# Optimization experiments

Hardware: AMD Instinct MI355X
Metric: run time of the kernel (lower is better)

## Reference

```python
import jax, jax.numpy as jnp
import numpy as np

P = 256        # number of graph pairs
LMAX = 32      # max graph size (padded to LMAX+1 incl. virtual node)
F = 2048       # num_input_features
E = 256        # embedding_dim
INF = 10000.0


def _lengths():
    i = np.arange(P)
    len_s = 8 + (i % 25)
    len_t = 8 + ((7 * i + 3) % 25)
    return len_s.astype(np.int32), len_t.astype(np.int32)


def setup_inputs() -> dict:
    key = jax.random.key(0)
    ks = jax.random.split(key, 6)
    len_s_np, len_t_np = _lengths()
    Ns, Nt = int(len_s_np.sum()), int(len_t_np.sum())
    x_s = jax.random.normal(ks[0], (Ns, F), jnp.float32)
    x_t = jax.random.normal(ks[1], (Nt, F), jnp.float32)
    W1 = jax.random.normal(ks[2], (E, F), jnp.float32) / np.float32(np.sqrt(F))
    b1 = jnp.zeros((E,), jnp.float32)
    W2 = jax.random.normal(ks[3], (E, E), jnp.float32) / np.float32(np.sqrt(E))
    b2 = jnp.zeros((E,), jnp.float32)
    virtual_embedding = jax.random.uniform(ks[4], (F,), jnp.float32)
    return {"x_s": x_s, "x_t": x_t, "W1": W1, "b1": b1, "W2": W2, "b2": b2,
            "virtual_embedding": virtual_embedding,
            "len_s": jnp.asarray(len_s_np), "len_t": jnp.asarray(len_t_np)}


def _embed(x, W1, b1, W2, b2):
    # nn.Sequential(Linear, Dropout(eval=identity), ReLU, Linear, ReLU)
    h = jax.nn.relu(x @ W1.T + b1)
    return jax.nn.relu(h @ W2.T + b2)


def _safe_cdist(a, b):
    # a: [P,L,E], b: [P,L,E] -> [P,L,L] Euclidean, grad-safe at 0
    sq = (jnp.sum(a * a, -1)[:, :, None] + jnp.sum(b * b, -1)[:, None, :]
          - 2.0 * jnp.einsum('pid,pjd->pij', a, b))
    sq = jnp.maximum(sq, 0.0)
    pos = sq > 0
    return jnp.where(pos, jnp.sqrt(jnp.where(pos, sq, 1.0)), 0.0)


def _pad_embed(emb, virtual_e, lens):
    # ragged [N,E] -> padded [P,LMAX+1,E]; slot lens[p] (and beyond) = virtual
    pos = jnp.arange(LMAX + 1)
    off = jnp.cumsum(lens) - lens                       # exclusive prefix sum
    idx = off[:, None] + jnp.minimum(pos[None, :], lens[:, None] - 1)
    mask = pos[None, :] < lens[:, None]
    return jnp.where(mask[..., None], emb[idx], virtual_e[None, None, :])


def _edit_costs(x_s, x_t, W1, b1, W2, b2, virtual_embedding, len_s, len_t):
    emb_s = _embed(x_s, W1, b1, W2, b2)
    emb_t = _embed(x_t, W1, b1, W2, b2)
    ve = _embed(virtual_embedding[None, :], W1, b1, W2, b2)[0]
    A = _pad_embed(emb_s, ve, len_s)                    # [P,L+1,E]
    B = _pad_embed(emb_t, ve, len_t)
    d = _safe_cdist(A, B)                               # [P,L+1,L+1]
    pos = jnp.arange(LMAX + 1)
    valid = ((pos[None, :, None] <= len_s[:, None, None]) &
             (pos[None, None, :] <= len_t[:, None, None]))
    tot = jnp.sum(jnp.where(valid, d, 0.0), axis=(1, 2))
    scale = (len_s * len_t).astype(d.dtype) / tot
    return jnp.where(valid, d * scale[:, None, None], 0.0), valid


def _lap_jv(C):
    # Jonker-Volgenant / e-maxx Hungarian for square cost matrix; returns col of each row
    C = np.asarray(C, dtype=np.float64)
    n = C.shape[0]
    u = np.zeros(n + 1)
    v = np.zeros(n + 1)
    p = np.zeros(n + 1, dtype=np.int64)
    way = np.zeros(n + 1, dtype=np.int64)
    for i in range(1, n + 1):
        p[0] = i
        j0 = 0
        minv = np.full(n + 1, np.inf)
        used = np.zeros(n + 1, dtype=bool)
        while True:
            used[j0] = True
            i0 = p[j0]
            cur = C[i0 - 1, :] - u[i0] - v[1:]
            upd = (~used[1:]) & (cur < minv[1:])
            minv[1:][upd] = cur[upd]
            way[1:][upd] = j0
            masked = np.where(used[1:], np.inf, minv[1:])
            j1 = int(np.argmin(masked)) + 1
            delta = masked[j1 - 1]
            u[p[used]] += delta
            v[used] -= delta
            minv[1:][~used[1:]] -= delta
            j0 = j1
            if p[j0] == 0:
                break
        while j0:
            j1 = way[j0]
            p[j0] = p[j1]
            j0 = j1
    row_of_col = p[1:] - 1
    col_of_row = np.empty(n, dtype=np.int64)
    col_of_row[row_of_col] = np.arange(n)
    return col_of_row


def _lsape_align(ec, n, m):
    # LSAPE expansion identical to GEDModelHomology.lsape
    N = n + m
    C = np.zeros((N, N))
    C[:n, :m] = ec[:n, :m]
    C[n:, :m] = INF
    C[:n, m:] = INF
    C[np.arange(n, n + m), np.arange(m)] = ec[n, :m]
    C[np.arange(n), np.arange(m, m + n)] = ec[:n, m]
    C[~np.isfinite(C)] = INF
    p = _lap_jv(C)
    q = np.arange(N)
    align = np.zeros((n + 1, m + 1), dtype=np.int32)
    align[np.minimum(q, n), np.minimum(p, m)] = 1
    align[-1, -1] = 0
    return align


def _alignments(costs_np, len_s_np, len_t_np):
    out = np.zeros((costs_np.shape[0], LMAX + 1, LMAX + 1), dtype=np.int32)
    for pr in range(costs_np.shape[0]):
        n, m = int(len_s_np[pr]), int(len_t_np[pr])
        out[pr, :n + 1, :m + 1] = _lsape_align(costs_np[pr, :n + 1, :m + 1], n, m)
    return out


def reference(x_s, x_t, W1, b1, W2, b2, virtual_embedding, len_s, len_t):
    costs, _ = _edit_costs(x_s, x_t, W1, b1, W2, b2, virtual_embedding, len_s, len_t)
    aligns = jnp.asarray(_alignments(np.asarray(costs),
                                     np.asarray(len_s), np.asarray(len_t)))
    geds = (jnp.sum(aligns.astype(costs.dtype) * costs, axis=(1, 2))
            / (len_s + len_t).astype(costs.dtype))
    return aligns, costs, geds
```

## Files before the change

### kernel.cpp

```cpp
#include <hip/hip_runtime.h>
#include <math.h>

#define LMAXP1 33
#define EDIM   256
#define FBIG   3.0e38f

typedef _Float16 half8 __attribute__((ext_vector_type(8)));
typedef float    f32x4 __attribute__((ext_vector_type(4)));

__device__ inline unsigned pk2h(_Float16 a, _Float16 b) {
    union { _Float16 h[2]; unsigned u; } q; q.h[0] = a; q.h[1] = b; return q.u;
}

#define ASTR 20
__global__ __launch_bounds__(256)
void k_gemm_splitk(const float* __restrict__ S0, int n0,
                   const float* __restrict__ S1, int n1,
                   const float* __restrict__ S2,
                   const float* __restrict__ W,
                   float* __restrict__ Part, int Mtot, int K, int kchunk,
                   const float* __restrict__ bias) {
    __shared__ alignas(16) unsigned AsH[64 * ASTR],  AsL[64 * ASTR];
    __shared__ alignas(16) unsigned BsH[256 * ASTR], BsL[256 * ASTR];
    const int tid = threadIdx.x;
    const int m0  = blockIdx.x * 64;
    const int ks  = blockIdx.z;
    const int kb  = ks * kchunk;
    const int ke  = (kb + kchunk < K) ? kb + kchunk : K;

    const int sar = tid >> 2, sak = (tid & 3) << 3;
    const int gr  = m0 + sar;
    const float* srow = nullptr;
    if (gr < n0)            srow = S0 + (size_t)gr * K;
    else if (gr < n0 + n1)  srow = S1 + (size_t)(gr - n0) * K;
    else if (gr < Mtot)     srow = S2;

    const int lane = tid & 63, wv = tid >> 6;
    const int wc = wv << 6;
    const int lr = lane & 15, lq = lane >> 4;

    f32x4 acc[4][4] = {};

    for (int k0 = kb; k0 < ke; k0 += 32) {
        {
            float x[8];
            if (srow) {
                const float4 f0 = *(const float4*)(srow + k0 + sak + 0);
                const float4 f1 = *(const float4*)(srow + k0 + sak + 4);
                x[0]=f0.x; x[1]=f0.y; x[2]=f0.z; x[3]=f0.w;
                x[4]=f1.x; x[5]=f1.y; x[6]=f1.z; x[7]=f1.w;
            } else {
                #pragma unroll
                for (int j = 0; j < 8; ++j) x[j] = 0.f;
            }
            unsigned uh[4], ul[4];
            #pragma unroll
            for (int j = 0; j < 4; ++j) {
                const _Float16 h0 = (_Float16)x[2*j],   h1 = (_Float16)x[2*j+1];
                const _Float16 l0 = (_Float16)(x[2*j]   - (float)h0);
                const _Float16 l1 = (_Float16)(x[2*j+1] - (float)h1);
                uh[j] = pk2h(h0, h1); ul[j] = pk2h(l0, l1);
            }
            *(uint4*)(AsH + sar * ASTR + (sak >> 1)) = make_uint4(uh[0],uh[1],uh[2],uh[3]);
            *(uint4*)(AsL + sar * ASTR + (sak >> 1)) = make_uint4(ul[0],ul[1],ul[2],ul[3]);
        }
        #pragma unroll
        for (int it = 0; it < 4; ++it) {
            const int idx = tid + it * 256;
            const int br = idx >> 2, bk = (idx & 3) << 3;
            const float* wr_ = W + (size_t)br * K + k0 + bk;
            const float4 f0 = *(const float4*)(wr_ + 0);
            const float4 f1 = *(const float4*)(wr_ + 4);
            const float y[8] = {f0.x,f0.y,f0.z,f0.w,f1.x,f1.y,f1.z,f1.w};
            unsigned uh[4], ul[4];
            #pragma unroll
            for (int j = 0; j < 4; ++j) {
                const float a0 = y[2*j] * 1024.0f, a1 = y[2*j+1] * 1024.0f;
                const _Float16 h0 = (_Float16)a0, h1 = (_Float16)a1;
                const _Float16 l0 = (_Float16)(a0 - (float)h0);
                const _Float16 l1 = (_Float16)(a1 - (float)h1);
                uh[j] = pk2h(h0, h1); ul[j] = pk2h(l0, l1);
            }
            *(uint4*)(BsH + br * ASTR + (bk >> 1)) = make_uint4(uh[0],uh[1],uh[2],uh[3]);
            *(uint4*)(BsL + br * ASTR + (bk >> 1)) = make_uint4(ul[0],ul[1],ul[2],ul[3]);
        }
        __syncthreads();

        half8 bhv[4], blv[4];
        #pragma unroll
        for (int ct = 0; ct < 4; ++ct) {
            const int br = wc + ct * 16 + lr;
            bhv[ct] = *(const half8*)((const char*)BsH + br * 80 + lq * 16);
            blv[ct] = *(const half8*)((const char*)BsL + br * 80 + lq * 16);
        }
        #pragma unroll
        for (int rt = 0; rt < 4; ++rt) {
            const int ar = rt * 16 + lr;
            const half8 ah = *(const half8*)((const char*)AsH + ar * 80 + lq * 16);
            const half8 al = *(const half8*)((const char*)AsL + ar * 80 + lq * 16);
            #pragma unroll
            for (int ct = 0; ct < 4; ++ct) {
                acc[rt][ct] = __builtin_amdgcn_mfma_f32_16x16x32_f16(ah, bhv[ct], acc[rt][ct], 0, 0, 0);
                acc[rt][ct] = __builtin_amdgcn_mfma_f32_16x16x32_f16(ah, blv[ct], acc[rt][ct], 0, 0, 0);
                acc[rt][ct] = __builtin_amdgcn_mfma_f32_16x16x32_f16(al, bhv[ct], acc[rt][ct], 0, 0, 0);
            }
        }
        __syncthreads();
    }

    float* pout = Part + (size_t)ks * ((size_t)Mtot * EDIM);
    const float sc = 1.0f / 1024.0f;
    #pragma unroll
    for (int rt = 0; rt < 4; ++rt) {
        #pragma unroll
        for (int r = 0; r < 4; ++r) {
            const int grr = m0 + rt * 16 + lq * 4 + r;
            if (grr >= Mtot) continue;
            #pragma unroll
            for (int ct = 0; ct < 4; ++ct) {
                const int gc = wc + ct * 16 + lr;
                float vv = acc[rt][ct][r] * sc;
                if (bias) vv = fmaxf(vv + bias[gc], 0.0f);
                pout[(size_t)grr * EDIM + gc] = vv;
            }
        }
    }
}

__global__ __launch_bounds__(256)
void k_reduce_bias_relu(const float* __restrict__ Part,
                        const float* __restrict__ bias,
                        float* __restrict__ C, int S, size_t MN4) {
    const size_t i = (size_t)blockIdx.x * blockDim.x + threadIdx.x;
    const size_t stride = (size_t)gridDim.x * blockDim.x;
    const size_t MN = MN4 * 4;
    for (size_t i4 = i; i4 < MN4; i4 += stride) {
        float4 s = ((const float4*)Part)[i4];
        for (int z = 1; z < S; ++z)
            { const float4 q = ((const float4*)(Part + (size_t)z * MN))[i4];
              s.x += q.x; s.y += q.y; s.z += q.z; s.w += q.w; }
        const float4 b = ((const float4*)bias)[i4 & 63];
        s.x = fmaxf(s.x + b.x, 0.f); s.y = fmaxf(s.y + b.y, 0.f);
        s.z = fmaxf(s.z + b.z, 0.f); s.w = fmaxf(s.w + b.w, 0.f);
        ((float4*)C)[i4] = s;
    }
}

__global__ __launch_bounds__(256)
void k_embed_gemm(const float* __restrict__ S0, int n0,
                  const float* __restrict__ S1, int n1,
                  const float* __restrict__ S2,
                  const float* __restrict__ W, const float* __restrict__ bias,
                  float* __restrict__ C, int Mtot, int K) {
    __shared__ alignas(16) float As[16][68];
    __shared__ alignas(16) float Bs[16][68];
    const int tid  = threadIdx.x;
    const int tx   = tid & 15, ty = tid >> 4;
    const int m0   = blockIdx.x * 64, nc0 = blockIdx.y * 64;
    const int lrow = tid >> 2;
    const int lk4  = (tid & 3) << 2;

    const int gr = m0 + lrow;
    const float* srow = nullptr;
    if (gr < n0)            srow = S0 + (size_t)gr * K;
    else if (gr < n0 + n1)  srow = S1 + (size_t)(gr - n0) * K;
    else if (gr < Mtot)     srow = S2;
    const float* wrow = W + (size_t)(nc0 + lrow) * K;

    float acc[4][4] = {};
    for (int k0 = 0; k0 < K; k0 += 16) {
        float4 va = make_float4(0.f, 0.f, 0.f, 0.f);
        if (srow) va = *(const float4*)(srow + k0 + lk4);
        const float4 vb = *(const float4*)(wrow + k0 + lk4);
        As[lk4+0][lrow] = va.x; As[lk4+1][lrow] = va.y;
        As[lk4+2][lrow] = va.z; As[lk4+3][lrow] = va.w;
        Bs[lk4+0][lrow] = vb.x; Bs[lk4+1][lrow] = vb.y;
        Bs[lk4+2][lrow] = vb.z; Bs[lk4+3][lrow] = vb.w;
        __syncthreads();
        #pragma unroll
        for (int kk = 0; kk < 16; ++kk) {
            const float4 a4 = *(const float4*)&As[kk][ty << 2];
            const float4 b4 = *(const float4*)&Bs[kk][tx << 2];
            const float av[4] = {a4.x, a4.y, a4.z, a4.w};
            const float bv[4] = {b4.x, b4.y, b4.z, b4.w};
            #pragma unroll
            for (int i2 = 0; i2 < 4; ++i2)
                #pragma unroll
                for (int j2 = 0; j2 < 4; ++j2)
                    acc[i2][j2] = fmaf(av[i2], bv[j2], acc[i2][j2]);
        }
        __syncthreads();
    }
    #pragma unroll
    for (int i2 = 0; i2 < 4; ++i2) {
        const int grr = m0 + (ty << 2) + i2;
        if (grr >= Mtot) continue;
        #pragma unroll
        for (int j2 = 0; j2 < 4; ++j2) {
            const int gc = nc0 + (tx << 2) + j2;
            const float vv = acc[i2][j2] + bias[gc];
            C[(size_t)grr * EDIM + gc] = fmaxf(vv, 0.0f);
        }
    }
}

#define CSTR 36
__global__ __launch_bounds__(256)
void k_costs(const float* __restrict__ Emb, const int* __restrict__ len_s,
             const int* __restrict__ len_t, int Ns, int Nt,
             float* __restrict__ costs) {
    __shared__ alignas(16) unsigned Ah[34 * CSTR], Al[34 * CSTR];
    __shared__ alignas(16) unsigned Bh[34 * CSTR], Bl[34 * CSTR];
    __shared__ float dtile[LMAXP1 * LMAXP1];
    __shared__ float na[LMAXP1], nb[LMAXP1];
    __shared__ float red[256];
    __shared__ float s_scale;
    const int p = blockIdx.x, tid = threadIdx.x;
    const int n = len_s[p], m = len_t[p];
    int offs = 0, offt = 0;
    for (int j = 0; j < p; ++j) { offs += len_s[j]; offt += len_t[j]; }
    const int veRow = Ns + Nt;
    const int tbase = Ns + offt;

    const int lane = tid & 63, wv = tid >> 6;
    const int lr = lane & 15, lq = lane >> 4;

    if (tid <= n) {
        const float* src = (tid < n) ? (Emb + (size_t)(offs + tid) * EDIM)
                                     : (Emb + (size_t)veRow * EDIM);
        const float4* a4 = (const float4*)src;
        float s = 0.f;
        for (int k = 0; k < 64; ++k) {
            const float4 a = a4[k];
            s = fmaf(a.x, a.x, s); s = fmaf(a.y, a.y, s);
            s = fmaf(a.z, a.z, s); s = fmaf(a.w, a.w, s);
        }
        na[tid] = s;
    } else if (tid >= 64 && tid - 64 <= m) {
        const int j = tid - 64;
        const float* src = (j < m) ? (Emb + (size_t)(tbase + j) * EDIM)
                                   : (Emb + (size_t)veRow * EDIM);
        const float4* b4 = (const float4*)src;
        float s = 0.f;
        for (int k = 0; k < 64; ++k) {
            const float4 b = b4[k];
            s = fmaf(b.x, b.x, s); s = fmaf(b.y, b.y, s);
            s = fmaf(b.z, b.z, s); s = fmaf(b.w, b.w, s);
        }
        nb[j] = s;
    }

    f32x4 g0 = {}, g1 = {}, g2 = {};
    const int t0 = wv, t1 = wv + 4, t2 = wv + 8;

    for (int k0 = 0; k0 < EDIM; k0 += 64) {
        for (int idx = tid; idx < 34 * 16; idx += 256) {
            const int r = idx >> 4, c4 = idx & 15;
            float4 va = make_float4(0.f,0.f,0.f,0.f), vb = va;
            if (r < n)       va = *(const float4*)(Emb + (size_t)(offs + r) * EDIM + k0 + c4*4);
            else if (r == n) va = *(const float4*)(Emb + (size_t)veRow * EDIM + k0 + c4*4);
            if (r < m)       vb = *(const float4*)(Emb + (size_t)(tbase + r) * EDIM + k0 + c4*4);
            else if (r == m) vb = *(const float4*)(Emb + (size_t)veRow * EDIM + k0 + c4*4);
            const float xa[4] = {va.x, va.y, va.z, va.w};
            const float xb[4] = {vb.x, vb.y, vb.z, vb.w};
            unsigned ah_[2], al_[2], bh_[2], bl_[2];
            #pragma unroll
            for (int j = 0; j < 2; ++j) {
                const _Float16 h0 = (_Float16)xa[2*j],   h1 = (_Float16)xa[2*j+1];
                const _Float16 l0 = (_Float16)(xa[2*j]   - (float)h0);
                const _Float16 l1 = (_Float16)(xa[2*j+1] - (float)h1);
                ah_[j] = pk2h(h0, h1); al_[j] = pk2h(l0, l1);
                const _Float16 g0_ = (_Float16)xb[2*j],   g1_ = (_Float16)xb[2*j+1];
                const _Float16 m0_ = (_Float16)(xb[2*j]   - (float)g0_);
                const _Float16 m1_ = (_Float16)(xb[2*j+1] - (float)g1_);
                bh_[j] = pk2h(g0_, g1_); bl_[j] = pk2h(m0_, m1_);
            }
            const int uo = r * CSTR + c4 * 2;
            *(uint2*)(Ah + uo) = make_uint2(ah_[0], ah_[1]);
            *(uint2*)(Al + uo) = make_uint2(al_[0], al_[1]);
            *(uint2*)(Bh + uo) = make_uint2(bh_[0], bh_[1]);
            *(uint2*)(Bl + uo) = make_uint2(bl_[0], bl_[1]);
        }
        __syncthreads();

        #pragma unroll
        for (int kf = 0; kf < 2; ++kf) {
#define GRAM_TILE(T, G) { \
            const int tr_ = (T) / 3, tc_ = (T) % 3;                              \
            const int ar_ = tr_ * 16 + lr, br_ = tc_ * 16 + lr;                  \
            const half8 ah = *(const half8*)((const char*)Ah + ar_*144 + kf*64 + lq*16); \
            const half8 al = *(const half8*)((const char*)Al + ar_*144 + kf*64 + lq*16); \
            const half8 bh = *(const half8*)((const char*)Bh + br_*144 + kf*64 + lq*16); \
            const half8 bl = *(const half8*)((const char*)Bl + br_*144 + kf*64 + lq*16); \
            G = __builtin_amdgcn_mfma_f32_16x16x32_f16(ah, bh, G, 0, 0, 0);      \
            G = __builtin_amdgcn_mfma_f32_16x16x32_f16(ah, bl, G, 0, 0, 0);      \
            G = __builtin_amdgcn_mfma_f32_16x16x32_f16(al, bh, G, 0, 0, 0); }
            GRAM_TILE(t0, g0)
            GRAM_TILE(t1, g1)
            if (wv == 0) GRAM_TILE(t2, g2)
#undef GRAM_TILE
        }
        __syncthreads();
    }

#define DTILE_OUT(T, G) { \
    const int tr_ = (T) / 3, tc_ = (T) % 3;                                      \
    _Pragma("unroll")                                                            \
    for (int r = 0; r < 4; ++r) {                                                \
        const int i_ = tr_ * 16 + lq * 4 + r, j_ = tc_ * 16 + lr;                \
        if (i_ <= n && j_ <= m) {                                                \
            const float sq = fmaxf(na[i_] + nb[j_] - 2.0f * G[r], 0.0f);         \
            dtile[i_ * LMAXP1 + j_] = (sq > 0.0f) ? sqrtf(sq) : 0.0f;            \
        } } }
    DTILE_OUT(t0, g0)
    DTILE_OUT(t1, g1)
    if (wv == 0) DTILE_OUT(t2, g2)
#undef DTILE_OUT
    __syncthreads();

    float lsum = 0.f;
    const int m1 = m + 1;
    const int cells = (n + 1) * m1;
    for (int c = tid; c < cells; c += 256) {
        const int i = c / m1, j = c - i * m1;
        lsum += dtile[i * LMAXP1 + j];
    }
    red[tid] = lsum;
    __syncthreads();
    for (int s = 128; s > 0; s >>= 1) {
        if (tid < s) red[tid] += red[tid + s];
        __syncthreads();
    }
    if (tid == 0) s_scale = (float)(n * m) / red[0];
    __syncthreads();
    const float scale = s_scale;
    for (int idx = tid; idx < LMAXP1 * LMAXP1; idx += 256) {
        const int i = idx / LMAXP1, j = idx - i * LMAXP1;
        const float v = (i <= n && j <= m) ? dtile[i * LMAXP1 + j] * scale : 0.0f;
        costs[(size_t)p * (LMAXP1 * LMAXP1) + idx] = v;
    }
}

__device__ inline int rdlane_i(int v, int l) { return __builtin_amdgcn_readlane(v, l); }
__device__ inline float rdlane_f(float v, int l) {
    return __int_as_float(__builtin_amdgcn_readlane(__float_as_int(v), l));
}
__device__ inline unsigned wave_umin64(unsigned x) {
#define DPPMINU(ctrl) { unsigned t_ = (unsigned)__builtin_amdgcn_update_dpp(  \
        (int)x, (int)x, (ctrl), 0xf, 0xf, false);                             \
        x = (t_ < x) ? t_ : x; }
    DPPMINU(0xB1)
    DPPMINU(0x4E)
    DPPMINU(0x141)
    DPPMINU(0x140)
    DPPMINU(0x142)
    DPPMINU(0x143)
#undef DPPMINU
    return (unsigned)__builtin_amdgcn_readlane((int)x, 63);
}

__global__ __launch_bounds__(64)
void k_lap(const float* __restrict__ costs, const int* __restrict__ len_s,
           const int* __restrict__ len_t, float* __restrict__ aligns,
           float* __restrict__ geds) {
    __shared__ float ec[LMAXP1 * LMAXP1];
    __shared__ float Ms[33 * 64];
    const int p = blockIdx.x, lane = threadIdx.x;
    const int n = len_s[p], m = len_t[p];
    const float* cp = costs + (size_t)p * (LMAXP1 * LMAXP1);
    for (int idx = lane; idx < LMAXP1 * LMAXP1; idx += 64) ec[idx] = cp[idx];
    __syncthreads();

    const bool swp = (n > m);
    const int R  = swp ? n : m;
    const int S_ = swp ? m : n;
    const bool vec = (lane >= 1 && lane <= R);

    for (int r = 1; r <= R; ++r) {
        float cv = FBIG;
        const int i0b = r - 1, j0b = lane - 1;
        if (vec) {
            if (!swp) {
                const float ins = ec[n * LMAXP1 + j0b];
                cv = (i0b < S_)
                   ? fminf(ec[i0b * LMAXP1 + j0b], ec[i0b * LMAXP1 + m] + ins)
                   : ins;
            } else {
                const float ins = ec[j0b * LMAXP1 + m];
                cv = (i0b < S_)
                   ? fminf(ec[j0b * LMAXP1 + i0b], ec[n * LMAXP1 + i0b] + ins)
                   : ins;
            }
        }
        Ms[(r << 6) + lane] = cv;
    }
    __syncthreads();

    float v_l = 0.0f;
    int amin_l = 0;
    if (vec) {
        float best = FBIG;
        for (int r = 1; r <= R; ++r) {
            const float c = Ms[(r << 6) + lane];
            if (c < best) { best = c; amin_l = r; }
        }
        v_l = best;
    }
    int p_l = 0;
    unsigned long long rowfree = ((1ull << R) - 1ull) << 1;
    for (int j = 1; j <= R; ++j) {
        const int ai = rdlane_i(amin_l, j);
        if ((rowfree >> ai) & 1ull) {
            if (lane == j) p_l = ai;
            rowfree &= ~(1ull << ai);
        }
    }

    float ucol = 0.0f, minv_l = FBIG;
    int way_l = 0;

    for (int i = 1; i <= R; ++i) {
        if (!((rowfree >> i) & 1ull)) continue;
        if (lane == 0) { p_l = i; ucol = 0.0f; }
        minv_l = FBIG;
        int used_l = 0;
        int j0 = 0, i0 = i;
        float u_i0 = 0.0f;
        while (true) {
            if (lane == j0) used_l = 1;
            const float cur = Ms[(i0 << 6) + lane] - u_i0 - v_l;
            const bool unused = vec && !used_l;
            if (unused && cur < minv_l) { minv_l = cur; way_l = j0; }
            const float mval = unused ? fmaxf(minv_l, 0.0f) : FBIG;
            const unsigned key = (__float_as_uint(mval) & ~63u) | (unsigned)lane;
            const unsigned kmin = wave_umin64(key);
            const int j1 = (int)(kmin & 63u);
            const float delta = rdlane_f(minv_l, j1);
            if (used_l) { ucol += delta; v_l -= delta; }
            if (unused) minv_l -= delta;
            j0 = j1;
            i0 = rdlane_i(p_l, j1);
            u_i0 = rdlane_f(ucol, j1);
            if (i0 == 0) break;
        }
        int jj = j0;
        while (jj != 0) {
            const int   j1a = rdlane_i(way_l, jj);
            const int   pn  = rdlane_i(p_l, j1a);
            const float un  = rdlane_f(ucol, j1a);
            if (lane == jj) { p_l = pn; ucol = un; }
            jj = j1a;
        }
    }

    float* ap = aligns + (size_t)p * (LMAXP1 * LMAXP1);
    for (int idx = lane; idx < LMAXP1 * LMAXP1; idx += 64) ap[idx] = 0.0f;
    __syncthreads();
    float gedv = 0.0f;
    if (vec) {
        const int i0b = p_l - 1;
        const int j0b = lane - 1;
        if (!swp) {
            if (i0b < S_) {
                const float sub = ec[i0b * LMAXP1 + j0b];
                const float alt = ec[i0b * LMAXP1 + m] + ec[n * LMAXP1 + j0b];
                if (sub <= alt) { ap[i0b * LMAXP1 + j0b] = 1.0f; gedv = sub; }
                else { ap[i0b * LMAXP1 + m] = 1.0f;
                       ap[n * LMAXP1 + j0b] = 1.0f;
                       gedv = alt; }
            } else {
                ap[n * LMAXP1 + j0b] = 1.0f;
                gedv = ec[n * LMAXP1 + j0b];
            }
        } else {
            if (i0b < S_) {
                const float sub = ec[j0b * LMAXP1 + i0b];
                const float alt = ec[n * LMAXP1 + i0b] + ec[j0b * LMAXP1 + m];
                if (sub <= alt) { ap[j0b * LMAXP1 + i0b] = 1.0f; gedv = sub; }
                else { ap[n * LMAXP1 + i0b] = 1.0f;
                       ap[j0b * LMAXP1 + m] = 1.0f;
                       gedv = alt; }
            } else {
                ap[j0b * LMAXP1 + m] = 1.0f;
                gedv = ec[j0b * LMAXP1 + m];
            }
        }
    }
    #pragma unroll
    for (int off = 32; off > 0; off >>= 1) gedv += __shfl_xor(gedv, off);
    if (lane == 0) geds[p] = gedv / (float)(n + m);
}

extern "C" void kernel_launch(void* const* d_in, const int* in_sizes, int n_in,
                              void* d_out, int out_size, void* d_ws, size_t ws_size,
                              hipStream_t stream) {
    const float* x_s = (const float*)d_in[0];
    const float* x_t = (const float*)d_in[1];
    const float* W1  = (const float*)d_in[2];
    const float* b1  = (const float*)d_in[3];
    const float* W2  = (const float*)d_in[4];
    const float* b2  = (const float*)d_in[5];
    const float* ve  = (const float*)d_in[6];
    const int* len_s = (const int*)d_in[7];
    const int* len_t = (const int*)d_in[8];
    const int P    = in_sizes[7];
    const int Ns   = in_sizes[0] / 2048;
    const int Nt   = in_sizes[1] / 2048;
    const int Mtot = Ns + Nt + 1;
    const size_t MN  = (size_t)Mtot * EDIM;

    float* H    = (float*)d_ws;
    float* Emb  = H + MN;
    float* Part = Emb + MN;

    int S = 1;
    if (ws_size >= (2 + 4) * MN * sizeof(float)) S = 4;
    else if (ws_size >= (2 + 2) * MN * sizeof(float)) S = 2;

    float* out_aligns = (float*)d_out;
    float* out_costs  = out_aligns + (size_t)P * LMAXP1 * LMAXP1;
    float* out_geds   = out_costs  + (size_t)P * LMAXP1 * LMAXP1;

    const dim3 b256(256);
    const int gx64 = (Mtot + 63) / 64;

    if (S > 1) {
        k_gemm_splitk<<<dim3(gx64, 1, S), b256, 0, stream>>>(
            x_s, Ns, x_t, Nt, ve, W1, Part, Mtot, 2048, 2048 / S, nullptr);
        const size_t MN4 = MN / 4;
        const int rblocks = (int)((MN4 + 255) / 256) < 2048
                          ? (int)((MN4 + 255) / 256) : 2048;
        k_reduce_bias_relu<<<dim3(rblocks), b256, 0, stream>>>(Part, b1, H, S, MN4);
        k_gemm_splitk<<<dim3(gx64, 1, 1), b256, 0, stream>>>(
            H, Mtot, nullptr, 0, nullptr, W2, Emb, Mtot, 256, 256, b2);
    } else {
        k_embed_gemm<<<dim3(gx64, 4), b256, 0, stream>>>(
            x_s, Ns, x_t, Nt, ve, W1, b1, H, Mtot, 2048);
        k_embed_gemm<<<dim3(gx64, 4), b256, 0, stream>>>(
            H, Mtot, nullptr, 0, nullptr, W2, b2, Emb, Mtot, 256);
    }
    k_costs<<<dim3(P), b256, 0, stream>>>(Emb, len_s, len_t, Ns, Nt, out_costs);
    k_lap<<<dim3(P), dim3(64), 0, stream>>>(out_costs, len_s, len_t, out_aligns, out_geds);
}
```

Before: 180.1 us.

## Pre-split weights and hidden activations into fp16 hi/lo buffers before GEMMs

Adds a conversion kernel that splits W1 and W2 once per call into packed fp16 high/low halves. The split-K GEMM now loads these directly instead of converting weights inside every block. The reduce kernel also emits the hidden layer as fp16 hi/lo, so a new dedicated GEMM for layer 2 consumes it without reconverting. This removes redundant per-block conversion work at the cost of two extra launches and extra workspace traffic.

```diff
diff --git a/kernel.cpp b/kernel.cpp
--- a/kernel.cpp
+++ b/kernel.cpp
@@ -10,6 +10,19 @@
 
 __device__ inline unsigned pk2h(_Float16 a, _Float16 b) {
     union { _Float16 h[2]; unsigned u; } q; q.h[0] = a; q.h[1] = b; return q.u;
+}
+
+__global__ __launch_bounds__(256)
+void k_convw(const float* __restrict__ W, unsigned* __restrict__ Wh,
+             unsigned* __restrict__ Wl, int npairs) {
+    const int stride = gridDim.x * blockDim.x;
+    for (int i = blockIdx.x * blockDim.x + threadIdx.x; i < npairs; i += stride) {
+        const float a0 = W[2*i] * 1024.0f, a1 = W[2*i+1] * 1024.0f;
+        const _Float16 h0 = (_Float16)a0, h1 = (_Float16)a1;
+        const _Float16 l0 = (_Float16)(a0 - (float)h0);
+        const _Float16 l1 = (_Float16)(a1 - (float)h1);
+        Wh[i] = pk2h(h0, h1); Wl[i] = pk2h(l0, l1);
+    }
 }
 
 #define ASTR 20
@@ -17,9 +30,8 @@
 void k_gemm_splitk(const float* __restrict__ S0, int n0,
                    const float* __restrict__ S1, int n1,
                    const float* __restrict__ S2,
-                   const float* __restrict__ W,
-                   float* __restrict__ Part, int Mtot, int K, int kchunk,
-                   const float* __restrict__ bias) {
+                   const unsigned* __restrict__ Wh, const unsigned* __restrict__ Wl,
+                   float* __restrict__ Part, int Mtot, int K, int kchunk) {
     __shared__ alignas(16) unsigned AsH[64 * ASTR],  AsL[64 * ASTR];
     __shared__ alignas(16) unsigned BsH[256 * ASTR], BsL[256 * ASTR];
     const int tid = threadIdx.x;
@@ -68,21 +80,9 @@
         for (int it = 0; it < 4; ++it) {
             const int idx = tid + it * 256;
             const int br = idx >> 2, bk = (idx & 3) << 3;
-            const float* wr_ = W + (size_t)br * K + k0 + bk;
-            const float4 f0 = *(const float4*)(wr_ + 0);
-            const float4 f1 = *(const float4*)(wr_ + 4);
-            const float y[8] = {f0.x,f0.y,f0.z,f0.w,f1.x,f1.y,f1.z,f1.w};
-            unsigned uh[4], ul[4];
-            #pragma unroll
-            for (int j = 0; j < 4; ++j) {
-                const float a0 = y[2*j] * 1024.0f, a1 = y[2*j+1] * 1024.0f;
-                const _Float16 h0 = (_Float16)a0, h1 = (_Float16)a1;
-                const _Float16 l0 = (_Float16)(a0 - (float)h0);
-                const _Float16 l1 = (_Float16)(a1 - (float)h1);
-                uh[j] = pk2h(h0, h1); ul[j] = pk2h(l0, l1);
-            }
-            *(uint4*)(BsH + br * ASTR + (bk >> 1)) = make_uint4(uh[0],uh[1],uh[2],uh[3]);
-            *(uint4*)(BsL + br * ASTR + (bk >> 1)) = make_uint4(ul[0],ul[1],ul[2],ul[3]);
+            const size_t uoff = (size_t)br * (K >> 1) + ((k0 + bk) >> 1);
+            *(uint4*)(BsH + br * ASTR + (bk >> 1)) = *(const uint4*)(Wh + uoff);
+            *(uint4*)(BsL + br * ASTR + (bk >> 1)) = *(const uint4*)(Wl + uoff);
         }
         __syncthreads();
 
@@ -117,12 +117,8 @@
             const int grr = m0 + rt * 16 + lq * 4 + r;
             if (grr >= Mtot) continue;
             #pragma unroll
-            for (int ct = 0; ct < 4; ++ct) {
-                const int gc = wc + ct * 16 + lr;
-                float vv = acc[rt][ct][r] * sc;
-                if (bias) vv = fmaxf(vv + bias[gc], 0.0f);
-                pout[(size_t)grr * EDIM + gc] = vv;
-            }
+            for (int ct = 0; ct < 4; ++ct)
+                pout[(size_t)grr * EDIM + wc + ct * 16 + lr] = acc[rt][ct][r] * sc;
         }
     }
 }
@@ -130,7 +126,8 @@
 __global__ __launch_bounds__(256)
 void k_reduce_bias_relu(const float* __restrict__ Part,
                         const float* __restrict__ bias,
-                        float* __restrict__ C, int S, size_t MN4) {
+                        unsigned* __restrict__ Hh, unsigned* __restrict__ Hl,
+                        int S, size_t MN4) {
     const size_t i = (size_t)blockIdx.x * blockDim.x + threadIdx.x;
     const size_t stride = (size_t)gridDim.x * blockDim.x;
     const size_t MN = MN4 * 4;
@@ -142,7 +139,91 @@
         const float4 b = ((const float4*)bias)[i4 & 63];
         s.x = fmaxf(s.x + b.x, 0.f); s.y = fmaxf(s.y + b.y, 0.f);
         s.z = fmaxf(s.z + b.z, 0.f); s.w = fmaxf(s.w + b.w, 0.f);
-        ((float4*)C)[i4] = s;
+        const _Float16 hx = (_Float16)s.x, hy = (_Float16)s.y;
+        const _Float16 hz = (_Float16)s.z, hw = (_Float16)s.w;
+        Hh[i4*2+0] = pk2h(hx, hy);
+        Hh[i4*2+1] = pk2h(hz, hw);
+        Hl[i4*2+0] = pk2h((_Float16)(s.x - (float)hx), (_Float16)(s.y - (float)hy));
+        Hl[i4*2+1] = pk2h((_Float16)(s.z - (float)hz), (_Float16)(s.w - (float)hw));
+    }
+}
+
+__global__ __launch_bounds__(256)
+void k_gemm_f16(const unsigned* __restrict__ Ah, const unsigned* __restrict__ Al,
+                const unsigned* __restrict__ Wh, const unsigned* __restrict__ Wl,
+                const float* __restrict__ bias,
+                float* __restrict__ C, int Mtot, int K) {
+    __shared__ alignas(16) unsigned AsH[64 * ASTR],  AsL[64 * ASTR];
+    __shared__ alignas(16) unsigned BsH[256 * ASTR], BsL[256 * ASTR];
+    const int tid = threadIdx.x;
+    const int m0  = blockIdx.x * 64;
+
+    const int sar = tid >> 2, sak = (tid & 3) << 3;
+    const int gr  = m0 + sar;
+    const bool arow = (gr < Mtot);
+
+    const int lane = tid & 63, wv = tid >> 6;
+    const int wc = wv << 6;
+    const int lr = lane & 15, lq = lane >> 4;
+
+    f32x4 acc[4][4] = {};
+
+    for (int k0 = 0; k0 < K; k0 += 32) {
+        {
+            uint4 vh = make_uint4(0,0,0,0), vl = vh;
+            if (arow) {
+                const size_t uoff = (size_t)gr * (K >> 1) + ((k0 + sak) >> 1);
+                vh = *(const uint4*)(Ah + uoff);
+                vl = *(const uint4*)(Al + uoff);
+            }
+            *(uint4*)(AsH + sar * ASTR + (sak >> 1)) = vh;
+            *(uint4*)(AsL + sar * ASTR + (sak >> 1)) = vl;
+        }
+        #pragma unroll
+        for (int it = 0; it < 4; ++it) {
+            const int idx = tid + it * 256;
+            const int br = idx >> 2, bk = (idx & 3) << 3;
+            const size_t uoff = (size_t)br * (K >> 1) + ((k0 + bk) >> 1);
+            *(uint4*)(BsH + br * ASTR + (bk >> 1)) = *(const uint4*)(Wh + uoff);
+            *(uint4*)(BsL + br * ASTR + (bk >> 1)) = *(const uint4*)(Wl + uoff);
+        }
+        __syncthreads();
+
+        half8 bhv[4], blv[4];
+        #pragma unroll
+        for (int ct = 0; ct < 4; ++ct) {
+            const int br = wc + ct * 16 + lr;
+            bhv[ct] = *(const half8*)((const char*)BsH + br * 80 + lq * 16);
+            blv[ct] = *(const half8*)((const char*)BsL + br * 80 + lq * 16);
+        }
+        #pragma unroll
+        for (int rt = 0; rt < 4; ++rt) {
+            const int ar = rt * 16 + lr;
+            const half8 ah = *(const half8*)((const char*)AsH + ar * 80 + lq * 16);
+            const half8 al = *(const half8*)((const char*)AsL + ar * 80 + lq * 16);
+            #pragma unroll
+            for (int ct = 0; ct < 4; ++ct) {
+                acc[rt][ct] = __builtin_amdgcn_mfma_f32_16x16x32_f16(ah, bhv[ct], acc[rt][ct], 0, 0, 0);
+                acc[rt][ct] = __builtin_amdgcn_mfma_f32_16x16x32_f16(ah, blv[ct], acc[rt][ct], 0, 0, 0);
+                acc[rt][ct] = __builtin_amdgcn_mfma_f32_16x16x32_f16(al, bhv[ct], acc[rt][ct], 0, 0, 0);
+            }
+        }
+        __syncthreads();
+    }
+
+    const float sc = 1.0f / 1024.0f;
+    #pragma unroll
+    for (int rt = 0; rt < 4; ++rt) {
+        #pragma unroll
+        for (int r = 0; r < 4; ++r) {
+            const int grr = m0 + rt * 16 + lq * 4 + r;
+            if (grr >= Mtot) continue;
+            #pragma unroll
+            for (int ct = 0; ct < 4; ++ct) {
+                const int gc = wc + ct * 16 + lr;
+                C[(size_t)grr * EDIM + gc] = fmaxf(acc[rt][ct][r] * sc + bias[gc], 0.0f);
+            }
+        }
     }
 }
 
@@ -509,14 +590,6 @@
     const int Mtot = Ns + Nt + 1;
     const size_t MN  = (size_t)Mtot * EDIM;
 
-    float* H    = (float*)d_ws;
-    float* Emb  = H + MN;
-    float* Part = Emb + MN;
-
-    int S = 1;
-    if (ws_size >= (2 + 4) * MN * sizeof(float)) S = 4;
-    else if (ws_size >= (2 + 2) * MN * sizeof(float)) S = 2;
-
     float* out_aligns = (float*)d_out;
     float* out_costs  = out_aligns + (size_t)P * LMAXP1 * LMAXP1;
     float* out_geds   = out_costs  + (size_t)P * LMAXP1 * LMAXP1;
@@ -524,21 +597,44 @@
     const dim3 b256(256);
     const int gx64 = (Mtot + 63) / 64;
 
-    if (S > 1) {
+    const size_t fixed = MN  + 2 * 262144 + 2 * 32768;
+    int S = 0;
+    if (ws_size >= (4 * MN + fixed) * sizeof(float)) S = 4;
+    else if (ws_size >= (2 * MN + fixed) * sizeof(float)) S = 2;
+
+    if (S > 0) {
+        float* Part = (float*)d_ws;
+        float* Emb  = Part;
+        unsigned* Hh  = (unsigned*)(Part + (size_t)S * MN);
+        unsigned* Hl  = Hh + MN / 2;
+        unsigned* W1h = Hl + MN / 2;
+        unsigned* W1l = W1h + 262144;
+        unsigned* W2h = W1l + 262144;
+        unsigned* W2l = W2h + 32768;
+
+        k_convw<<<dim3(1024), b256, 0, stream>>>(W1, W1h, W1l, 262144);
+        k_convw<<<dim3(128),  b256, 0, stream>>>(W2, W2h, W2l, 32768);
+
         k_gemm_splitk<<<dim3(gx64, 1, S), b256, 0, stream>>>(
-            x_s, Ns, x_t, Nt, ve, W1, Part, Mtot, 2048, 2048 / S, nullptr);
+            x_s, Ns, x_t, Nt, ve, W1h, W1l, Part, Mtot, 2048, 2048 / S);
+
         const size_t MN4 = MN / 4;
         const int rblocks = (int)((MN4 + 255) / 256) < 2048
                           ? (int)((MN4 + 255) / 256) : 2048;
-        k_reduce_bias_relu<<<dim3(rblocks), b256, 0, stream>>>(Part, b1, H, S, MN4);
-        k_gemm_splitk<<<dim3(gx64, 1, 1), b256, 0, stream>>>(
-            H, Mtot, nullptr, 0, nullptr, W2, Emb, Mtot, 256, 256, b2);
+        k_reduce_bias_relu<<<dim3(rblocks), b256, 0, stream>>>(Part, b1, Hh, Hl, S, MN4);
+
+        k_gemm_f16<<<dim3(gx64), b256, 0, stream>>>(Hh, Hl, W2h, W2l, b2, Emb, Mtot, 256);
+
+        k_costs<<<dim3(P), b256, 0, stream>>>(Emb, len_s, len_t, Ns, Nt, out_costs);
+        k_lap<<<dim3(P), dim3(64), 0, stream>>>(out_costs, len_s, len_t, out_aligns, out_geds);
     } else {
+        float* H   = (float*)d_ws;
+        float* Emb = H + MN;
         k_embed_gemm<<<dim3(gx64, 4), b256, 0, stream>>>(
             x_s, Ns, x_t, Nt, ve, W1, b1, H, Mtot, 2048);
         k_embed_gemm<<<dim3(gx64, 4), b256, 0, stream>>>(
             H, Mtot, nullptr, 0, nullptr, W2, b2, Emb, Mtot, 256);
-    }
-    k_costs<<<dim3(P), b256, 0, stream>>>(Emb, len_s, len_t, Ns, Nt, out_costs);
-    k_lap<<<dim3(P), dim3(64), 0, stream>>>(out_costs, len_s, len_t, out_aligns, out_geds);
-}
+        k_costs<<<dim3(P), b256, 0, stream>>>(Emb, len_s, len_t, Ns, Nt, out_costs);
+        k_lap<<<dim3(P), dim3(64), 0, stream>>>(out_costs, len_s, len_t, out_aligns, out_geds);
+    }
+}
```

Measured after the change: 174.9 us. 2.9% less time.
